# Optimization experiments

Hardware: AMD Instinct MI355X
Metric: run time of the kernel (lower is better)

Reference implementation:

```python
import jax, jax.numpy as jnp
import numpy as np

K = 16          # knn neighbors (init kwarg k)
GROUPS = 4      # GroupNorm groups
EPS = 1e-5
SLOPE = 0.2     # LeakyReLU negative slope


def fps(xyz, n):
    """Farthest point sampling. xyz: (B,N,3) -> idx (B,n). First index is 0 (pointnet2 convention)."""
    B, N, _ = xyz.shape

    def step(carry, _):
        dist, last = carry
        p = jnp.take_along_axis(xyz, last[:, None, None], axis=1)  # (B,1,3)
        d = jnp.sum((xyz - p) ** 2, axis=-1)                       # (B,N)
        dist = jnp.minimum(dist, d)
        nxt = jnp.argmax(dist, axis=-1).astype(jnp.int32)
        return (dist, nxt), nxt

    init = (jnp.full((B, N), jnp.inf, xyz.dtype), jnp.zeros((B,), jnp.int32))
    _, idxs = jax.lax.scan(step, init, None, length=n - 1)  # (n-1, B)
    return jnp.concatenate([jnp.zeros((B, 1), jnp.int32), idxs.T], axis=1)


def graph_feature(cq, fq, ck, fk):
    """DGCNN edge features. cq:(B,Q,3) fq:(B,Q,C) ck:(B,N,3) fk:(B,N,C) -> (B,Q,K,2C)."""
    d2 = (jnp.sum(cq * cq, -1)[:, :, None]
          - 2.0 * jnp.einsum('bqc,bnc->bqn', cq, ck)
          + jnp.sum(ck * ck, -1)[:, None, :])        # (B,Q,N)
    _, idx = jax.lax.top_k(-d2, K)                    # (B,Q,K) nearest first
    nb = jax.vmap(lambda f_, i_: f_[i_])(fk, idx)     # (B,Q,K,C)
    ctr = jnp.broadcast_to(fq[:, :, None, :], nb.shape)
    return jnp.concatenate([nb - ctr, ctr], axis=-1)


def conv_gn_lrelu(y, W, gw, gb):
    """1x1 Conv2d (no bias) + GroupNorm(4) + LeakyReLU(0.2). y: (B,Q,K,Cin), W: (Cout,Cin)."""
    y = jnp.einsum('bqkc,oc->bqko', y, W)
    B, Q, Kk, C = y.shape
    yg = y.reshape(B, Q * Kk, GROUPS, C // GROUPS)
    m = yg.mean(axis=(1, 3), keepdims=True)
    v = yg.var(axis=(1, 3), keepdims=True)
    y = ((yg - m) * jax.lax.rsqrt(v + EPS)).reshape(B, Q, Kk, C) * gw + gb
    return jnp.where(y > 0, y, SLOPE * y)


def setup_inputs() -> dict:
    key = jax.random.key(0)
    ks = jax.random.split(key, 16)
    B, N = 8, 4096
    s = lambda k_, shape, scale=0.1: (jax.random.normal(k_, shape, jnp.float32) * scale)
    return {
        'x': jax.random.normal(ks[0], (B, N, 7), jnp.float32),
        'W_in': s(ks[1], (8, 3), 0.5), 'b_in': s(ks[2], (8,), 0.02),
        'W1': s(ks[3], (32, 16), 0.2), 'g1w': jnp.ones((32,), jnp.float32), 'g1b': jnp.zeros((32,), jnp.float32),
        'W2': s(ks[4], (64, 64), 0.1), 'g2w': jnp.ones((64,), jnp.float32), 'g2b': jnp.zeros((64,), jnp.float32),
        'W3': s(ks[5], (64, 128), 0.1), 'g3w': jnp.ones((64,), jnp.float32), 'g3b': jnp.zeros((64,), jnp.float32),
        'W4': s(ks[6], (128, 128), 0.1), 'g4w': jnp.ones((128,), jnp.float32), 'g4b': jnp.zeros((128,), jnp.float32),
        'num0': 1024,
    }


def reference(x, W_in, b_in, W1, g1w, g1b, W2, g2w, g2b, W3, g3w, g3b, W4, g4w, g4b, num0):
    coor, normal, plane = x[..., :3], x[..., 3:6], x[..., 6:7]   # (B,N,3),(B,N,3),(B,N,1)

    # input_trans: Conv1d(3,8,1)
    f = jnp.einsum('bnc,oc->bno', coor, W_in) + b_in             # (B,N,8)

    g = graph_feature(coor, f, coor, f)                          # (B,N,K,16)
    f = conv_gn_lrelu(g, W1, g1w, g1b).max(axis=2)               # (B,N,32)

    idx = fps(coor, num0)
    gather = lambda a: jnp.take_along_axis(a, idx[:, :, None], axis=1)
    coor_q, normal_q, plane_q, f_q = gather(coor), gather(normal), gather(plane), gather(f)

    g = graph_feature(coor_q, f_q, coor, f)                      # (B,num0,K,64)
    f = conv_gn_lrelu(g, W2, g2w, g2b).max(axis=2)               # (B,num0,64)
    coor, normal, plane = coor_q, normal_q, plane_q

    g = graph_feature(coor, f, coor, f)                          # (B,num0,K,128)
    f = conv_gn_lrelu(g, W3, g3w, g3b).max(axis=2)               # (B,num0,64)

    idx = fps(coor, num0)  # source uses num[0] again
    gather = lambda a: jnp.take_along_axis(a, idx[:, :, None], axis=1)
    coor_q, normal_q, plane_q, f_q = gather(coor), gather(normal), gather(plane), gather(f)

    g = graph_feature(coor_q, f_q, coor, f)                      # (B,num0,K,128)
    f = conv_gn_lrelu(g, W4, g4w, g4b).max(axis=2)               # (B,num0,128)

    return coor_q, f, normal_q, plane_q
```

## Files before the change

kernel.cpp:

```cpp
#include <hip/hip_runtime.h>
#include <cstdint>

static constexpr int B   = 8;
static constexpr int N0  = 4096;
static constexpr int NQ  = 1024;
static constexpr int KNB = 16;

__device__ __forceinline__ unsigned long long wave_max_u64_l63(unsigned long long k) {
#define STEPU_(ctrl)                                                                    \
  {                                                                                     \
    unsigned lo_ = (unsigned)k, hi_ = (unsigned)(k >> 32);                              \
    unsigned plo_ = (unsigned)__builtin_amdgcn_update_dpp((int)lo_, (int)lo_, ctrl,     \
                                                          0xf, 0xf, false);             \
    unsigned phi_ = (unsigned)__builtin_amdgcn_update_dpp((int)hi_, (int)hi_, ctrl,     \
                                                          0xf, 0xf, false);             \
    unsigned long long pk_ = ((unsigned long long)phi_ << 32) | plo_;                   \
    if (pk_ > k) k = pk_;                                                               \
  }
  STEPU_(0x111) STEPU_(0x112) STEPU_(0x114) STEPU_(0x118) STEPU_(0x142) STEPU_(0x143)
#undef STEPU_
  return k;
}

__global__ void prep_kernel(const float* __restrict__ x,
                            const float* __restrict__ W_in,
                            const float* __restrict__ b_in,
                            float4* __restrict__ c4, float* __restrict__ nrm,
                            float* __restrict__ pl, float* __restrict__ f0) {
  int i = blockIdx.x * 256 + threadIdx.x;
  if (i >= B * N0) return;
  const float* xp = x + (size_t)i * 7;
  float cx = xp[0], cy = xp[1], cz = xp[2];
  float kk = __fadd_rn(__fadd_rn(__fmul_rn(cx, cx), __fmul_rn(cy, cy)), __fmul_rn(cz, cz));
  c4[i] = make_float4(cx, cy, cz, kk);
  nrm[i * 3 + 0] = xp[3]; nrm[i * 3 + 1] = xp[4]; nrm[i * 3 + 2] = xp[5];
  pl[i] = xp[6];
#pragma unroll
  for (int o = 0; o < 8; o++) {
    f0[(size_t)i * 8 + o] = cx * W_in[o * 3 + 0] + cy * W_in[o * 3 + 1] + cz * W_in[o * 3 + 2] + b_in[o];
  }
}

template <int NC>
__device__ __forceinline__ void knn_body(int bq, int lane,
                                         const float4* __restrict__ q4,
                                         const float4* __restrict__ k4,
                                         int Q, int Nk, int* __restrict__ out) {
  int b = bq / Q;
  float4 q = q4[bq];
  const float4* kb = k4 + (size_t)b * Nk + lane;
  const float INF    = __int_as_float(0x7f800000);
  const float NEGINF = __int_as_float(0xff800000);
  float myd = INF;
  int   myi = 0;
  float kth = INF;
  const bool isl0 = (lane & 15) == 0;
  constexpr int G = (NC >= 8) ? 8 : NC;
  for (int c0 = 0; c0 < NC; c0 += G) {
    float dg[G];
#pragma unroll
    for (int u = 0; u < G; u++) {
      float4 kp = kb[(c0 + u) * 64];
      float dot = __fadd_rn(__fadd_rn(__fmul_rn(q.x, kp.x), __fmul_rn(q.y, kp.y)),
                            __fmul_rn(q.z, kp.z));
      dg[u] = __fadd_rn(__fsub_rn(q.w, __fmul_rn(2.0f, dot)), kp.w);
    }
#pragma unroll
    for (int u = 0; u < G; u++) {
      float d = dg[u];
      unsigned long long m = __ballot(d < kth);
      while (m) {
        int j = __builtin_ctzll(m);
        float dv = __int_as_float(__builtin_amdgcn_readlane(__float_as_int(d), j));
        int   iv = (c0 + u) * 64 + j;
        bool gt = (myd > dv);
        float pd = __int_as_float(__builtin_amdgcn_update_dpp(
            0, __float_as_int(myd), 0x111, 0xf, 0xf, true));
        int   pi = __builtin_amdgcn_update_dpp(0, myi, 0x111, 0xf, 0xf, true);
        pd = isl0 ? NEGINF : pd;
        bool tp = (pd > dv);
        float nd = tp ? pd : dv;
        int   ni = tp ? pi : iv;
        myd = gt ? nd : myd;
        myi = gt ? ni : myi;
        kth = __int_as_float(__builtin_amdgcn_readlane(__float_as_int(myd), 15));
        m = __ballot(d < kth);
        m = (j < 63) ? (m & (~0ull << (j + 1))) : 0ull;
      }
    }
  }
  if (lane < KNB) out[(size_t)bq * KNB + lane] = myi;
}

template <int CF, int CO>
__device__ __forceinline__ void ctry_body(int i, int total, const float* __restrict__ fq,
                                          const float* __restrict__ W,
                                          float* __restrict__ ctrY,
                                          const int* __restrict__ ridx, int Q, int Nsrc) {
  if (i >= total) return;
  int o = i % CO, bq = i / CO;
  const float* fp;
  if (ridx) {
    int b = bq / Q;
    fp = fq + ((size_t)b * Nsrc + ridx[bq]) * CF;
  } else {
    fp = fq + (size_t)bq * CF;
  }
  const float* wp = W + (size_t)o * (2 * CF) + CF;
  float acc = 0.f;
#pragma unroll
  for (int c = 0; c < CF; c++) acc = fmaf(fp[c], wp[c], acc);
  ctrY[i] = acc;
}

template <int NPTS>
__device__ __forceinline__ void fps_body(const float4* __restrict__ cb, int* w) {
  constexpr int BLK = 256;
  constexpr int M = NPTS / BLK;
  constexpr int NW = BLK / 64;
  __shared__ __align__(16) float2 sxy[NPTS];
  __shared__ float szz[NPTS];
  __shared__ __align__(16) unsigned long long skey[2][NW];
  const int tid = threadIdx.x;
  const int wid = tid >> 6, lane = tid & 63;
  float cx[M], cy[M], cz[M], dist[M];
#pragma unroll
  for (int i = 0; i < M; i++) {
    float4 p = cb[tid * M + i];
    cx[i] = p.x; cy[i] = p.y; cz[i] = p.z;
    dist[i] = 3.4e38f;
    sxy[tid * M + i] = make_float2(p.x, p.y);
    szz[tid * M + i] = p.z;
  }
  w[0] = w[1] = w[2] = w[3] = 0;
  float4 p0 = cb[0];
  float px = p0.x, py = p0.y, pz = p0.z;
  __syncthreads();
  for (int t = 1; t < NQ; t++) {
    float bv = -1.f; int bi = 0;
#pragma unroll
    for (int i = 0; i < M; i++) {
      float dx = __fsub_rn(cx[i], px), dy = __fsub_rn(cy[i], py), dz = __fsub_rn(cz[i], pz);
      float d = __fadd_rn(__fadd_rn(__fmul_rn(dx, dx), __fmul_rn(dy, dy)), __fmul_rn(dz, dz));
      float dd = dist[i]; dd = (d < dd) ? d : dd; dist[i] = dd;
      if (dd > bv) { bv = dd; bi = tid * M + i; }
    }
    unsigned long long k =
        ((unsigned long long)__float_as_uint(bv) << 12) | (unsigned)(4095 - bi);
    k = wave_max_u64_l63(k);
    int p = t & 1;
    if (lane == 63) skey[p][wid] = k;
    __syncthreads();
    ulonglong2 ab = *(const ulonglong2*)&skey[p][0];
    ulonglong2 cd = *(const ulonglong2*)&skey[p][2];
    unsigned long long m0 = (ab.x > ab.y) ? ab.x : ab.y;
    unsigned long long m1 = (cd.x > cd.y) ? cd.x : cd.y;
    unsigned long long mk = (m0 > m1) ? m0 : m1;
    int win = 4095 - (int)(mk & 0xFFFull);
    float2 pxy = sxy[win];
    px = pxy.x; py = pxy.y; pz = szz[win];
    if (t == tid) w[0] = win;
    if (t == tid + 256) w[1] = win;
    if (t == tid + 512) w[2] = win;
    if (t == tid + 768) w[3] = win;
  }
}

__global__ __launch_bounds__(256, 2) void mega1_kernel(
    const float4* __restrict__ c40, const float* __restrict__ nrm,
    const float* __restrict__ pl, const float* __restrict__ f0,
    const float* __restrict__ W1, int* __restrict__ idx1,
    float4* __restrict__ c4q1, float* __restrict__ nq1, float* __restrict__ pq1,
    int* __restrict__ knn1, float* __restrict__ ctrY1) {
  int blk = blockIdx.x;
  if (blk < 8) {
    const int b = blk, tid = threadIdx.x;
    const float4* cb = c40 + (size_t)b * N0;
    int w[4];
    fps_body<N0>(cb, w);
    int* idxb = idx1 + (size_t)b * NQ;
#pragma unroll
    for (int u = 0; u < 4; u++) {
      int r = tid + u * 256;
      int s = (u == 0 && tid == 0) ? 0 : w[u];
      idxb[r] = s;
      c4q1[(size_t)b * NQ + r] = cb[s];
      const float* np = nrm + ((size_t)b * N0 + s) * 3;
      float* ndp = nq1 + ((size_t)b * NQ + r) * 3;
      ndp[0] = np[0]; ndp[1] = np[1]; ndp[2] = np[2];
      pq1[(size_t)b * NQ + r] = pl[(size_t)b * N0 + s];
    }
  } else if (blk < 8 + 8192) {
    int bq = (blk - 8) * 4 + (threadIdx.x >> 6);
    knn_body<64>(bq, threadIdx.x & 63, c40, c40, N0, N0, knn1);
  } else {
    int i = (blk - (8 + 8192)) * 256 + threadIdx.x;
    ctry_body<8, 32>(i, B * N0 * 32, f0, W1, ctrY1, nullptr, 0, 0);
  }
}

__global__ __launch_bounds__(256, 2) void mega2_kernel(
    const float4* __restrict__ c40, const float4* __restrict__ c4q1,
    const float* __restrict__ nq1, const float* __restrict__ pq1,
    const float* __restrict__ f1, const int* __restrict__ idx1,
    const float* __restrict__ W2, int* __restrict__ idx2,
    float4* __restrict__ c4q2, float* __restrict__ cq2out,
    float* __restrict__ nq2out, float* __restrict__ pq2out,
    int* __restrict__ knn2, int* __restrict__ knn3, float* __restrict__ ctrY2) {
  int blk = blockIdx.x;
  if (blk < 8) {
    const int b = blk, tid = threadIdx.x;
    const float4* cqb = c4q1 + (size_t)b * NQ;
    int w[4];
    fps_body<NQ>(cqb, w);
    int* idxb = idx2 + (size_t)b * NQ;
#pragma unroll
    for (int u = 0; u < 4; u++) {
      int r = tid + u * 256;
      int s = (u == 0 && tid == 0) ? 0 : w[u];
      idxb[r] = s;
      float4 c = cqb[s];
      c4q2[(size_t)b * NQ + r] = c;
      float* cd = cq2out + ((size_t)b * NQ + r) * 3;
      cd[0] = c.x; cd[1] = c.y; cd[2] = c.z;
      const float* np = nq1 + ((size_t)b * NQ + s) * 3;
      float* ndp = nq2out + ((size_t)b * NQ + r) * 3;
      ndp[0] = np[0]; ndp[1] = np[1]; ndp[2] = np[2];
      pq2out[(size_t)b * NQ + r] = pq1[(size_t)b * NQ + s];
    }
  } else if (blk < 8 + 2048) {
    int bq = (blk - 8) * 4 + (threadIdx.x >> 6);
    knn_body<64>(bq, threadIdx.x & 63, c4q1, c40, NQ, N0, knn2);
  } else if (blk < 8 + 4096) {
    int bq = (blk - (8 + 2048)) * 4 + (threadIdx.x >> 6);
    knn_body<16>(bq, threadIdx.x & 63, c4q1, c4q1, NQ, NQ, knn3);
  } else {
    int i = (blk - (8 + 4096)) * 256 + threadIdx.x;
    ctry_body<32, 64>(i, B * NQ * 64, f1, W2, ctrY2, idx1, NQ, N0);
  }
}

__global__ __launch_bounds__(256, 4) void mega3_kernel(
    const float4* __restrict__ c4q1, const float4* __restrict__ c4q2,
    const float* __restrict__ f3, const int* __restrict__ idx2,
    const float* __restrict__ W4, int* __restrict__ knn4, float* __restrict__ ctrY4) {
  int blk = blockIdx.x;
  if (blk < 2048) {
    int bq = blk * 4 + (threadIdx.x >> 6);
    knn_body<16>(bq, threadIdx.x & 63, c4q2, c4q1, NQ, NQ, knn4);
  } else {
    int i = (blk - 2048) * 256 + threadIdx.x;
    ctry_body<64, 128>(i, B * NQ * 128, f3, W4, ctrY4, idx2, NQ, NQ);
  }
}

template <int CF, int CO>
__global__ void ctry_kernel(const float* __restrict__ fq, const float* __restrict__ W,
                            float* __restrict__ ctrY, int total) {
  int i = blockIdx.x * 256 + threadIdx.x;
  ctry_body<CF, CO>(i, total, fq, W, ctrY, nullptr, 0, 0);
}

template <int CF, int CO>
__global__ __launch_bounds__(256) void edgeconv_kernel(
    const float* __restrict__ fq, const float* __restrict__ fk,
    const int* __restrict__ knn, const float* __restrict__ Wfull,
    const float* __restrict__ ctrY, const int* __restrict__ ridx,
    float* __restrict__ ymin, float* __restrict__ ymax,
    float* __restrict__ gstats, int Q, int Nk) {
  constexpr int J = CO / 4;
  constexpr int SEC = J * CF + 8;
  __shared__ float Wl[4 * SEC];
  __shared__ float sstat[8];
  for (int t = threadIdx.x; t < CO * CF; t += 256) {
    int o = t / CF, c = t % CF;
    Wl[(o / J) * SEC + (o % J) * CF + c] = Wfull[(size_t)o * (2 * CF) + c];
  }
  if (threadIdx.x < 8) sstat[threadIdx.x] = 0.0f;
  __syncthreads();
  const int wid = threadIdx.x >> 6, lane = threadIdx.x & 63;
  const int bq = blockIdx.x * 4 + wid;
  const int b = bq / Q;
  const int g = lane >> 4, k = lane & 15;
  const int ni = knn[(size_t)bq * KNB + k];
  const float* nbp = fk + (size_t)(b * Nk + ni) * CF;
  const float* cp = ridx ? fq + ((size_t)b * Nk + ridx[bq]) * CF
                         : fq + (size_t)bq * CF;
  float acc[J];
#pragma unroll
  for (int j = 0; j < J; j++) acc[j] = 0.0f;
  const float* wg = &Wl[g * SEC];
#pragma unroll
  for (int c = 0; c < CF; c += 4) {
    float4 nb4 = *(const float4*)(nbp + c);
    float4 c4  = *(const float4*)(cp + c);
    float e0 = nb4.x - c4.x, e1 = nb4.y - c4.y, e2 = nb4.z - c4.z, e3 = nb4.w - c4.w;
#pragma unroll
    for (int j = 0; j < J; j++) {
      float4 w4 = *(const float4*)(wg + j * CF + c);
      acc[j] = fmaf(e0, w4.x, acc[j]);
      acc[j] = fmaf(e1, w4.y, acc[j]);
      acc[j] = fmaf(e2, w4.z, acc[j]);
      acc[j] = fmaf(e3, w4.w, acc[j]);
    }
  }
  float s = 0.f, s2 = 0.f;
  const float* cyp = ctrY + (size_t)bq * CO + g * J;
#pragma unroll
  for (int j = 0; j < J; j++) {
    float y = acc[j] + cyp[j];
    acc[j] = y;
    s += y; s2 = fmaf(y, y, s2);
  }
  float mn[J];
#pragma unroll
  for (int j = 0; j < J; j++) mn[j] = acc[j];
#pragma unroll
  for (int m = 1; m < 16; m <<= 1) {
#pragma unroll
    for (int j = 0; j < J; j++) {
      float a = __shfl_xor(acc[j], m); if (a > acc[j]) acc[j] = a;
      float c2 = __shfl_xor(mn[j], m); if (c2 < mn[j]) mn[j] = c2;
    }
    s  += __shfl_xor(s, m);
    s2 += __shfl_xor(s2, m);
  }
  if (k == 0) {
    float* mnp = ymin + (size_t)bq * CO + g * J;
    float* mxp = ymax + (size_t)bq * CO + g * J;
#pragma unroll
    for (int j = 0; j < J; j++) { mnp[j] = mn[j]; mxp[j] = acc[j]; }
    atomicAdd(&sstat[g], s);
    atomicAdd(&sstat[4 + g], s2);
  }
  __syncthreads();
  if (threadIdx.x < 8) atomicAdd(&gstats[b * 8 + threadIdx.x], sstat[threadIdx.x]);
}

template <int CO>
__global__ void gn_out_kernel(const float* __restrict__ ymin, const float* __restrict__ ymax,
                              const float* __restrict__ gstats, const float* __restrict__ gw,
                              const float* __restrict__ gb, float* __restrict__ fout,
                              int total, int Q, float inv_cnt) {
  int i = blockIdx.x * 256 + threadIdx.x;
  if (i >= total) return;
  constexpr int J = CO / 4;
  int o = i % CO; int bq = i / CO; int b = bq / Q;
  int g = o / J;
  float m  = gstats[b * 8 + g] * inv_cnt;
  float s2 = gstats[b * 8 + 4 + g] * inv_cnt;
  float rs = rsqrtf(s2 - m * m + 1e-5f);
  float sc = gw[o] * rs;
  float sel = (sc >= 0.f) ? ymax[i] : ymin[i];
  float v = (sel - m) * sc + gb[o];
  fout[i] = (v > 0.f) ? v : 0.2f * v;
}

extern "C" void kernel_launch(void* const* d_in, const int* in_sizes, int n_in,
                              void* d_out, int out_size, void* d_ws, size_t ws_size,
                              hipStream_t stream) {
  (void)in_sizes; (void)n_in; (void)out_size; (void)ws_size;
  const float* x    = (const float*)d_in[0];
  const float* W_in = (const float*)d_in[1];
  const float* b_in = (const float*)d_in[2];
  const float* W1   = (const float*)d_in[3];
  const float* g1w  = (const float*)d_in[4];
  const float* g1b  = (const float*)d_in[5];
  const float* W2   = (const float*)d_in[6];
  const float* g2w  = (const float*)d_in[7];
  const float* g2b  = (const float*)d_in[8];
  const float* W3   = (const float*)d_in[9];
  const float* g3w  = (const float*)d_in[10];
  const float* g3b  = (const float*)d_in[11];
  const float* W4   = (const float*)d_in[12];
  const float* g4w  = (const float*)d_in[13];
  const float* g4b  = (const float*)d_in[14];

  float* ws = (float*)d_ws;
  size_t o_c40  = 0;
  size_t o_nrm  = o_c40  + (size_t)B * N0 * 4;
  size_t o_pl   = o_nrm  + (size_t)B * N0 * 3;
  size_t o_f0   = o_pl   + (size_t)B * N0;
  size_t o_f1   = o_f0   + (size_t)B * N0 * 8;
  size_t o_ctrY = o_f1   + (size_t)B * N0 * 32;
  size_t o_ymin = o_ctrY + (size_t)B * N0 * 32;
  size_t o_ymax = o_ymin + (size_t)B * N0 * 32;
  size_t o_knnA = o_ymax + (size_t)B * N0 * 32;
  size_t o_knnB = o_knnA + (size_t)B * N0 * KNB;
  size_t o_gst  = o_knnB + (size_t)B * NQ * KNB;
  size_t o_idx1 = o_gst  + 4 * B * 8;
  size_t o_idx2 = o_idx1 + (size_t)B * NQ;
  size_t o_c4q1 = o_idx2 + (size_t)B * NQ;
  size_t o_c4q2 = o_c4q1 + (size_t)B * NQ * 4;
  size_t o_nq1  = o_c4q2 + (size_t)B * NQ * 4;
  size_t o_pq1  = o_nq1  + (size_t)B * NQ * 3;
  size_t o_f2   = o_pq1  + (size_t)B * NQ;
  size_t o_f3   = o_f2   + (size_t)B * NQ * 64;

  float4* c40  = (float4*)(ws + o_c40);
  float*  nrm  = ws + o_nrm;   float* pl   = ws + o_pl;
  float*  f0   = ws + o_f0;    float* f1   = ws + o_f1;
  float*  ctrY = ws + o_ctrY;  float* ymin = ws + o_ymin;  float* ymax = ws + o_ymax;
  int*    knnA = (int*)(ws + o_knnA);
  int*    knnB = (int*)(ws + o_knnB);
  float*  gst  = ws + o_gst;
  int*    idx1 = (int*)(ws + o_idx1);
  int*    idx2 = (int*)(ws + o_idx2);
  float4* c4q1 = (float4*)(ws + o_c4q1);
  float4* c4q2 = (float4*)(ws + o_c4q2);
  float*  nq1  = ws + o_nq1;   float* pq1  = ws + o_pq1;
  float*  f2   = ws + o_f2;    float* f3   = ws + o_f3;

  float* out  = (float*)d_out;
  float* cq2  = out;
  float* fout = out + (size_t)B * NQ * 3;
  float* nq2  = fout + (size_t)B * NQ * 128;
  float* pq2  = nq2 + (size_t)B * NQ * 3;

  hipMemsetAsync(gst, 0, 4 * B * 8 * sizeof(float), stream);

  prep_kernel<<<(B * N0 + 255) / 256, 256, 0, stream>>>(x, W_in, b_in, c40, nrm, pl, f0);

  mega1_kernel<<<8 + 8192 + 4096, 256, 0, stream>>>(c40, nrm, pl, f0, W1,
                                                    idx1, c4q1, nq1, pq1, knnA, ctrY);
  edgeconv_kernel<8, 32><<<B * N0 / 4, 256, 0, stream>>>(f0, f0, knnA, W1, ctrY, nullptr,
                                                         ymin, ymax, gst + 0, N0, N0);
  gn_out_kernel<32><<<(B * N0 * 32 + 255) / 256, 256, 0, stream>>>(
      ymin, ymax, gst + 0, g1w, g1b, f1, B * N0 * 32, N0, 1.0f / (4096.0f * 16.0f * 8.0f));

  mega2_kernel<<<8 + 2048 + 2048 + 2048, 256, 0, stream>>>(
      c40, c4q1, nq1, pq1, f1, idx1, W2, idx2, c4q2, cq2, nq2, pq2, knnA, knnB, ctrY);
  edgeconv_kernel<32, 64><<<B * NQ / 4, 256, 0, stream>>>(f1, f1, knnA, W2, ctrY, idx1,
                                                          ymin, ymax, gst + B * 8, NQ, N0);
  gn_out_kernel<64><<<(B * NQ * 64 + 255) / 256, 256, 0, stream>>>(
      ymin, ymax, gst + B * 8, g2w, g2b, f2, B * NQ * 64, NQ, 1.0f / (1024.0f * 16.0f * 16.0f));

  ctry_kernel<64, 64><<<(B * NQ * 64 + 255) / 256, 256, 0, stream>>>(f2, W3, ctrY, B * NQ * 64);
  edgeconv_kernel<64, 64><<<B * NQ / 4, 256, 0, stream>>>(f2, f2, knnB, W3, ctrY, nullptr,
                                                          ymin, ymax, gst + 2 * B * 8, NQ, NQ);
  gn_out_kernel<64><<<(B * NQ * 64 + 255) / 256, 256, 0, stream>>>(
      ymin, ymax, gst + 2 * B * 8, g3w, g3b, f3, B * NQ * 64, NQ, 1.0f / (1024.0f * 16.0f * 16.0f));

  mega3_kernel<<<2048 + 4096, 256, 0, stream>>>(c4q1, c4q2, f3, idx2, W4, knnB, ctrY);
  edgeconv_kernel<64, 128><<<B * NQ / 4, 256, 0, stream>>>(f3, f3, knnB, W4, ctrY, idx2,
                                                           ymin, ymax, gst + 3 * B * 8, NQ, NQ);
  gn_out_kernel<128><<<(B * NQ * 128 + 255) / 256, 256, 0, stream>>>(
      ymin, ymax, gst + 3 * B * 8, g4w, g4b, fout, B * NQ * 128, NQ, 1.0f / (1024.0f * 16.0f * 32.0f));
}
```

Baseline: 1.508 ms.

## Batch FPS over multiple clouds per block, carry coords in reduction, move FPS2 earlier

FPS now processes two clouds per block (four for the second FPS), interleaving independent reductions so one barrier per iteration is shared across several batches. The winning point's coordinates travel through the DPP wave reduction, which removes the shared-memory point table and the dependent LDS lookup after each step. The second FPS moves out of mega2 and is fused with the first edgeconv launch, so it starts earlier and overlaps edgeconv1 and gn_out. In exchange, fewer blocks carry the serial FPS critical path, each with more registers and work per iteration.

```diff
diff --git a/kernel.cpp b/kernel.cpp
--- a/kernel.cpp
+++ b/kernel.cpp
@@ -6,20 +6,31 @@
 static constexpr int NQ  = 1024;
 static constexpr int KNB = 16;
 
-__device__ __forceinline__ unsigned long long wave_max_u64_l63(unsigned long long k) {
-#define STEPU_(ctrl)                                                                    \
-  {                                                                                     \
-    unsigned lo_ = (unsigned)k, hi_ = (unsigned)(k >> 32);                              \
-    unsigned plo_ = (unsigned)__builtin_amdgcn_update_dpp((int)lo_, (int)lo_, ctrl,     \
-                                                          0xf, 0xf, false);             \
-    unsigned phi_ = (unsigned)__builtin_amdgcn_update_dpp((int)hi_, (int)hi_, ctrl,     \
-                                                          0xf, 0xf, false);             \
-    unsigned long long pk_ = ((unsigned long long)phi_ << 32) | plo_;                   \
-    if (pk_ > k) k = pk_;                                                               \
-  }
-  STEPU_(0x111) STEPU_(0x112) STEPU_(0x114) STEPU_(0x118) STEPU_(0x142) STEPU_(0x143)
-#undef STEPU_
-  return k;
+__device__ __forceinline__ void wave_max_u64_xyz_l63(unsigned long long& k,
+                                                     float& x, float& y, float& z) {
+#define STEPP_(ctrl)                                                                     \
+  {                                                                                      \
+    unsigned lo_ = (unsigned)k, hi_ = (unsigned)(k >> 32);                               \
+    unsigned plo_ = (unsigned)__builtin_amdgcn_update_dpp((int)lo_, (int)lo_, ctrl,      \
+                                                          0xf, 0xf, false);              \
+    unsigned phi_ = (unsigned)__builtin_amdgcn_update_dpp((int)hi_, (int)hi_, ctrl,      \
+                                                          0xf, 0xf, false);              \
+    float px_ = __int_as_float(__builtin_amdgcn_update_dpp(__float_as_int(x),            \
+                                                           __float_as_int(x), ctrl,     \
+                                                           0xf, 0xf, false));            \
+    float py_ = __int_as_float(__builtin_amdgcn_update_dpp(__float_as_int(y),            \
+                                                           __float_as_int(y), ctrl,     \
+                                                           0xf, 0xf, false));            \
+    float pz_ = __int_as_float(__builtin_amdgcn_update_dpp(__float_as_int(z),            \
+                                                           __float_as_int(z), ctrl,     \
+                                                           0xf, 0xf, false));            \
+    unsigned long long pk_ = ((unsigned long long)phi_ << 32) | plo_;                    \
+    bool sw_ = pk_ > k;                                                                  \
+    k = sw_ ? pk_ : k;                                                                   \
+    x = sw_ ? px_ : x; y = sw_ ? py_ : y; z = sw_ ? pz_ : z;                             \
+  }
+  STEPP_(0x111) STEPP_(0x112) STEPP_(0x114) STEPP_(0x118) STEPP_(0x142) STEPP_(0x143)
+#undef STEPP_
 }
 
 __global__ void prep_kernel(const float* __restrict__ x,
@@ -113,57 +124,151 @@
   ctrY[i] = acc;
 }
 
-template <int NPTS>
-__device__ __forceinline__ void fps_body(const float4* __restrict__ cb, int* w) {
-  constexpr int BLK = 256;
-  constexpr int M = NPTS / BLK;
-  constexpr int NW = BLK / 64;
-  __shared__ __align__(16) float2 sxy[NPTS];
-  __shared__ float szz[NPTS];
-  __shared__ __align__(16) unsigned long long skey[2][NW];
+template <int NPTS, int BPB>
+__device__ __forceinline__ void fps_body_multi(const float4* __restrict__ cb,
+                                               int (&w)[BPB][4]) {
+  constexpr int M = NPTS / 256;
+  __shared__ __align__(16) unsigned long long skey[2][BPB][4];
+  __shared__ __align__(16) float4 spay[2][BPB][4];
   const int tid = threadIdx.x;
   const int wid = tid >> 6, lane = tid & 63;
-  float cx[M], cy[M], cz[M], dist[M];
-#pragma unroll
-  for (int i = 0; i < M; i++) {
-    float4 p = cb[tid * M + i];
-    cx[i] = p.x; cy[i] = p.y; cz[i] = p.z;
-    dist[i] = 3.4e38f;
-    sxy[tid * M + i] = make_float2(p.x, p.y);
-    szz[tid * M + i] = p.z;
-  }
-  w[0] = w[1] = w[2] = w[3] = 0;
-  float4 p0 = cb[0];
-  float px = p0.x, py = p0.y, pz = p0.z;
+  float cx[BPB][M], cy[BPB][M], cz[BPB][M], dist[BPB][M];
+  float px[BPB], py[BPB], pz[BPB];
+#pragma unroll
+  for (int bb = 0; bb < BPB; bb++) {
+#pragma unroll
+    for (int i = 0; i < M; i++) {
+      float4 p = cb[(size_t)bb * NPTS + tid * M + i];
+      cx[bb][i] = p.x; cy[bb][i] = p.y; cz[bb][i] = p.z;
+      dist[bb][i] = 3.4e38f;
+    }
+#pragma unroll
+    for (int u = 0; u < 4; u++) w[bb][u] = 0;
+    float4 p0 = cb[(size_t)bb * NPTS];
+    px[bb] = p0.x; py[bb] = p0.y; pz[bb] = p0.z;
+  }
+  for (int t = 1; t < NQ; t++) {
+    const int p = t & 1;
+#pragma unroll
+    for (int bb = 0; bb < BPB; bb++) {
+      float bv = -1.f; int bi = 0;
+      float bx = 0.f, by = 0.f, bz = 0.f;
+#pragma unroll
+      for (int i = 0; i < M; i++) {
+        float dx = __fsub_rn(cx[bb][i], px[bb]);
+        float dy = __fsub_rn(cy[bb][i], py[bb]);
+        float dz = __fsub_rn(cz[bb][i], pz[bb]);
+        float d = __fadd_rn(__fadd_rn(__fmul_rn(dx, dx), __fmul_rn(dy, dy)), __fmul_rn(dz, dz));
+        float dd = dist[bb][i]; dd = (d < dd) ? d : dd; dist[bb][i] = dd;
+        if (dd > bv) { bv = dd; bi = tid * M + i; bx = cx[bb][i]; by = cy[bb][i]; bz = cz[bb][i]; }
+      }
+      unsigned long long k =
+          ((unsigned long long)__float_as_uint(bv) << 12) | (unsigned)(4095 - bi);
+      wave_max_u64_xyz_l63(k, bx, by, bz);
+      if (lane == 63) {
+        skey[p][bb][wid] = k;
+        spay[p][bb][wid] = make_float4(bx, by, bz, 0.f);
+      }
+    }
+    __syncthreads();
+#pragma unroll
+    for (int bb = 0; bb < BPB; bb++) {
+      unsigned long long k0 = skey[p][bb][0], k1 = skey[p][bb][1];
+      unsigned long long k2 = skey[p][bb][2], k3 = skey[p][bb][3];
+      float4 q0 = spay[p][bb][0], q1 = spay[p][bb][1];
+      float4 q2 = spay[p][bb][2], q3 = spay[p][bb][3];
+      bool sA = k1 > k0;
+      unsigned long long ka = sA ? k1 : k0;
+      float xa = sA ? q1.x : q0.x, ya = sA ? q1.y : q0.y, za = sA ? q1.z : q0.z;
+      bool sB = k3 > k2;
+      unsigned long long kb2 = sB ? k3 : k2;
+      float xb = sB ? q3.x : q2.x, yb = sB ? q3.y : q2.y, zb = sB ? q3.z : q2.z;
+      bool sC = kb2 > ka;
+      unsigned long long kw = sC ? kb2 : ka;
+      px[bb] = sC ? xb : xa; py[bb] = sC ? yb : ya; pz[bb] = sC ? zb : za;
+      int win = 4095 - (int)(kw & 0xFFFull);
+      if (t == tid) w[bb][0] = win;
+      if (t == tid + 256) w[bb][1] = win;
+      if (t == tid + 512) w[bb][2] = win;
+      if (t == tid + 768) w[bb][3] = win;
+    }
+  }
+}
+
+template <int CF, int CO>
+__device__ __forceinline__ void edgeconv_body(
+    int blkid, const float* __restrict__ fq, const float* __restrict__ fk,
+    const int* __restrict__ knn, const float* __restrict__ Wfull,
+    const float* __restrict__ ctrY, const int* __restrict__ ridx,
+    float* __restrict__ ymin, float* __restrict__ ymax,
+    float* __restrict__ gstats, int Q, int Nk) {
+  constexpr int J = CO / 4;
+  constexpr int SEC = J * CF + 8;
+  __shared__ float Wl[4 * SEC];
+  __shared__ float sstat[8];
+  for (int t = threadIdx.x; t < CO * CF; t += 256) {
+    int o = t / CF, c = t % CF;
+    Wl[(o / J) * SEC + (o % J) * CF + c] = Wfull[(size_t)o * (2 * CF) + c];
+  }
+  if (threadIdx.x < 8) sstat[threadIdx.x] = 0.0f;
   __syncthreads();
-  for (int t = 1; t < NQ; t++) {
-    float bv = -1.f; int bi = 0;
-#pragma unroll
-    for (int i = 0; i < M; i++) {
-      float dx = __fsub_rn(cx[i], px), dy = __fsub_rn(cy[i], py), dz = __fsub_rn(cz[i], pz);
-      float d = __fadd_rn(__fadd_rn(__fmul_rn(dx, dx), __fmul_rn(dy, dy)), __fmul_rn(dz, dz));
-      float dd = dist[i]; dd = (d < dd) ? d : dd; dist[i] = dd;
-      if (dd > bv) { bv = dd; bi = tid * M + i; }
-    }
-    unsigned long long k =
-        ((unsigned long long)__float_as_uint(bv) << 12) | (unsigned)(4095 - bi);
-    k = wave_max_u64_l63(k);
-    int p = t & 1;
-    if (lane == 63) skey[p][wid] = k;
-    __syncthreads();
-    ulonglong2 ab = *(const ulonglong2*)&skey[p][0];
-    ulonglong2 cd = *(const ulonglong2*)&skey[p][2];
-    unsigned long long m0 = (ab.x > ab.y) ? ab.x : ab.y;
-    unsigned long long m1 = (cd.x > cd.y) ? cd.x : cd.y;
-    unsigned long long mk = (m0 > m1) ? m0 : m1;
-    int win = 4095 - (int)(mk & 0xFFFull);
-    float2 pxy = sxy[win];
-    px = pxy.x; py = pxy.y; pz = szz[win];
-    if (t == tid) w[0] = win;
-    if (t == tid + 256) w[1] = win;
-    if (t == tid + 512) w[2] = win;
-    if (t == tid + 768) w[3] = win;
-  }
+  const int wid = threadIdx.x >> 6, lane = threadIdx.x & 63;
+  const int bq = blkid * 4 + wid;
+  const int b = bq / Q;
+  const int g = lane >> 4, k = lane & 15;
+  const int ni = knn[(size_t)bq * KNB + k];
+  const float* nbp = fk + (size_t)(b * Nk + ni) * CF;
+  const float* cp = ridx ? fq + ((size_t)b * Nk + ridx[bq]) * CF
+                         : fq + (size_t)bq * CF;
+  float acc[J];
+#pragma unroll
+  for (int j = 0; j < J; j++) acc[j] = 0.0f;
+  const float* wg = &Wl[g * SEC];
+#pragma unroll
+  for (int c = 0; c < CF; c += 4) {
+    float4 nb4 = *(const float4*)(nbp + c);
+    float4 c4  = *(const float4*)(cp + c);
+    float e0 = nb4.x - c4.x, e1 = nb4.y - c4.y, e2 = nb4.z - c4.z, e3 = nb4.w - c4.w;
+#pragma unroll
+    for (int j = 0; j < J; j++) {
+      float4 w4 = *(const float4*)(wg + j * CF + c);
+      acc[j] = fmaf(e0, w4.x, acc[j]);
+      acc[j] = fmaf(e1, w4.y, acc[j]);
+      acc[j] = fmaf(e2, w4.z, acc[j]);
+      acc[j] = fmaf(e3, w4.w, acc[j]);
+    }
+  }
+  float s = 0.f, s2 = 0.f;
+  const float* cyp = ctrY + (size_t)bq * CO + g * J;
+#pragma unroll
+  for (int j = 0; j < J; j++) {
+    float y = acc[j] + cyp[j];
+    acc[j] = y;
+    s += y; s2 = fmaf(y, y, s2);
+  }
+  float mn[J];
+#pragma unroll
+  for (int j = 0; j < J; j++) mn[j] = acc[j];
+#pragma unroll
+  for (int m = 1; m < 16; m <<= 1) {
+#pragma unroll
+    for (int j = 0; j < J; j++) {
+      float a = __shfl_xor(acc[j], m); if (a > acc[j]) acc[j] = a;
+      float c2 = __shfl_xor(mn[j], m); if (c2 < mn[j]) mn[j] = c2;
+    }
+    s  += __shfl_xor(s, m);
+    s2 += __shfl_xor(s2, m);
+  }
+  if (k == 0) {
+    float* mnp = ymin + (size_t)bq * CO + g * J;
+    float* mxp = ymax + (size_t)bq * CO + g * J;
+#pragma unroll
+    for (int j = 0; j < J; j++) { mnp[j] = mn[j]; mxp[j] = acc[j]; }
+    atomicAdd(&sstat[g], s);
+    atomicAdd(&sstat[4 + g], s2);
+  }
+  __syncthreads();
+  if (threadIdx.x < 8) atomicAdd(&gstats[b * 8 + threadIdx.x], sstat[threadIdx.x]);
 }
 
 __global__ __launch_bounds__(256, 2) void mega1_kernel(
@@ -173,69 +278,94 @@
     float4* __restrict__ c4q1, float* __restrict__ nq1, float* __restrict__ pq1,
     int* __restrict__ knn1, float* __restrict__ ctrY1) {
   int blk = blockIdx.x;
-  if (blk < 8) {
-    const int b = blk, tid = threadIdx.x;
-    const float4* cb = c40 + (size_t)b * N0;
-    int w[4];
-    fps_body<N0>(cb, w);
-    int* idxb = idx1 + (size_t)b * NQ;
-#pragma unroll
-    for (int u = 0; u < 4; u++) {
-      int r = tid + u * 256;
-      int s = (u == 0 && tid == 0) ? 0 : w[u];
-      idxb[r] = s;
-      c4q1[(size_t)b * NQ + r] = cb[s];
-      const float* np = nrm + ((size_t)b * N0 + s) * 3;
-      float* ndp = nq1 + ((size_t)b * NQ + r) * 3;
-      ndp[0] = np[0]; ndp[1] = np[1]; ndp[2] = np[2];
-      pq1[(size_t)b * NQ + r] = pl[(size_t)b * N0 + s];
-    }
-  } else if (blk < 8 + 8192) {
-    int bq = (blk - 8) * 4 + (threadIdx.x >> 6);
+  if (blk < 4) {
+    const int tid = threadIdx.x;
+    const int b0 = blk * 2;
+    const float4* cb = c40 + (size_t)b0 * N0;
+    int w[2][4];
+    fps_body_multi<N0, 2>(cb, w);
+#pragma unroll
+    for (int bb = 0; bb < 2; bb++) {
+      const int b = b0 + bb;
+      const float4* cbb = c40 + (size_t)b * N0;
+      int* idxb = idx1 + (size_t)b * NQ;
+#pragma unroll
+      for (int u = 0; u < 4; u++) {
+        int r = tid + u * 256;
+        int s = (u == 0 && tid == 0) ? 0 : w[bb][u];
+        idxb[r] = s;
+        c4q1[(size_t)b * NQ + r] = cbb[s];
+        const float* np = nrm + ((size_t)b * N0 + s) * 3;
+        float* ndp = nq1 + ((size_t)b * NQ + r) * 3;
+        ndp[0] = np[0]; ndp[1] = np[1]; ndp[2] = np[2];
+        pq1[(size_t)b * NQ + r] = pl[(size_t)b * N0 + s];
+      }
+    }
+  } else if (blk < 4 + 8192) {
+    int bq = (blk - 4) * 4 + (threadIdx.x >> 6);
     knn_body<64>(bq, threadIdx.x & 63, c40, c40, N0, N0, knn1);
   } else {
-    int i = (blk - (8 + 8192)) * 256 + threadIdx.x;
+    int i = (blk - (4 + 8192)) * 256 + threadIdx.x;
     ctry_body<8, 32>(i, B * N0 * 32, f0, W1, ctrY1, nullptr, 0, 0);
+  }
+}
+
+__global__ __launch_bounds__(256) void ec1f_kernel(
+    const float4* __restrict__ c4q1, const float* __restrict__ nq1,
+    const float* __restrict__ pq1, const float* __restrict__ f0,
+    const int* __restrict__ knn1, const float* __restrict__ W1,
+    const float* __restrict__ ctrY1, float* __restrict__ ymin,
+    float* __restrict__ ymax, float* __restrict__ gst1,
+    int* __restrict__ idx2, float4* __restrict__ c4q2,
+    float* __restrict__ cq2out, float* __restrict__ nq2out,
+    float* __restrict__ pq2out) {
+  int blk = blockIdx.x;
+  if (blk < 2) {
+    const int tid = threadIdx.x;
+    const int b0 = blk * 4;
+    const float4* cqb = c4q1 + (size_t)b0 * NQ;
+    int w[4][4];
+    fps_body_multi<NQ, 4>(cqb, w);
+#pragma unroll
+    for (int bb = 0; bb < 4; bb++) {
+      const int b = b0 + bb;
+      const float4* cbb = c4q1 + (size_t)b * NQ;
+      int* idxb = idx2 + (size_t)b * NQ;
+#pragma unroll
+      for (int u = 0; u < 4; u++) {
+        int r = tid + u * 256;
+        int s = (u == 0 && tid == 0) ? 0 : w[bb][u];
+        idxb[r] = s;
+        float4 c = cbb[s];
+        c4q2[(size_t)b * NQ + r] = c;
+        float* cd = cq2out + ((size_t)b * NQ + r) * 3;
+        cd[0] = c.x; cd[1] = c.y; cd[2] = c.z;
+        const float* np = nq1 + ((size_t)b * NQ + s) * 3;
+        float* ndp = nq2out + ((size_t)b * NQ + r) * 3;
+        ndp[0] = np[0]; ndp[1] = np[1]; ndp[2] = np[2];
+        pq2out[(size_t)b * NQ + r] = pq1[(size_t)b * NQ + s];
+      }
+    }
+  } else {
+    edgeconv_body<8, 32>(blk - 2, f0, f0, knn1, W1, ctrY1, nullptr,
+                         ymin, ymax, gst1, N0, N0);
   }
 }
 
 __global__ __launch_bounds__(256, 2) void mega2_kernel(
     const float4* __restrict__ c40, const float4* __restrict__ c4q1,
-    const float* __restrict__ nq1, const float* __restrict__ pq1,
     const float* __restrict__ f1, const int* __restrict__ idx1,
-    const float* __restrict__ W2, int* __restrict__ idx2,
-    float4* __restrict__ c4q2, float* __restrict__ cq2out,
-    float* __restrict__ nq2out, float* __restrict__ pq2out,
+    const float* __restrict__ W2,
     int* __restrict__ knn2, int* __restrict__ knn3, float* __restrict__ ctrY2) {
   int blk = blockIdx.x;
-  if (blk < 8) {
-    const int b = blk, tid = threadIdx.x;
-    const float4* cqb = c4q1 + (size_t)b * NQ;
-    int w[4];
-    fps_body<NQ>(cqb, w);
-    int* idxb = idx2 + (size_t)b * NQ;
-#pragma unroll
-    for (int u = 0; u < 4; u++) {
-      int r = tid + u * 256;
-      int s = (u == 0 && tid == 0) ? 0 : w[u];
-      idxb[r] = s;
-      float4 c = cqb[s];
-      c4q2[(size_t)b * NQ + r] = c;
-      float* cd = cq2out + ((size_t)b * NQ + r) * 3;
-      cd[0] = c.x; cd[1] = c.y; cd[2] = c.z;
-      const float* np = nq1 + ((size_t)b * NQ + s) * 3;
-      float* ndp = nq2out + ((size_t)b * NQ + r) * 3;
-      ndp[0] = np[0]; ndp[1] = np[1]; ndp[2] = np[2];
-      pq2out[(size_t)b * NQ + r] = pq1[(size_t)b * NQ + s];
-    }
-  } else if (blk < 8 + 2048) {
-    int bq = (blk - 8) * 4 + (threadIdx.x >> 6);
+  if (blk < 2048) {
+    int bq = blk * 4 + (threadIdx.x >> 6);
     knn_body<64>(bq, threadIdx.x & 63, c4q1, c40, NQ, N0, knn2);
-  } else if (blk < 8 + 4096) {
-    int bq = (blk - (8 + 2048)) * 4 + (threadIdx.x >> 6);
+  } else if (blk < 4096) {
+    int bq = (blk - 2048) * 4 + (threadIdx.x >> 6);
     knn_body<16>(bq, threadIdx.x & 63, c4q1, c4q1, NQ, NQ, knn3);
   } else {
-    int i = (blk - (8 + 4096)) * 256 + threadIdx.x;
+    int i = (blk - 4096) * 256 + threadIdx.x;
     ctry_body<32, 64>(i, B * NQ * 64, f1, W2, ctrY2, idx1, NQ, N0);
   }
 }
@@ -268,73 +398,8 @@
     const float* __restrict__ ctrY, const int* __restrict__ ridx,
     float* __restrict__ ymin, float* __restrict__ ymax,
     float* __restrict__ gstats, int Q, int Nk) {
-  constexpr int J = CO / 4;
-  constexpr int SEC = J * CF + 8;
-  __shared__ float Wl[4 * SEC];
-  __shared__ float sstat[8];
-  for (int t = threadIdx.x; t < CO * CF; t += 256) {
-    int o = t / CF, c = t % CF;
-    Wl[(o / J) * SEC + (o % J) * CF + c] = Wfull[(size_t)o * (2 * CF) + c];
-  }
-  if (threadIdx.x < 8) sstat[threadIdx.x] = 0.0f;
-  __syncthreads();
-  const int wid = threadIdx.x >> 6, lane = threadIdx.x & 63;
-  const int bq = blockIdx.x * 4 + wid;
-  const int b = bq / Q;
-  const int g = lane >> 4, k = lane & 15;
-  const int ni = knn[(size_t)bq * KNB + k];
-  const float* nbp = fk + (size_t)(b * Nk + ni) * CF;
-  const float* cp = ridx ? fq + ((size_t)b * Nk + ridx[bq]) * CF
-                         : fq + (size_t)bq * CF;
-  float acc[J];
-#pragma unroll
-  for (int j = 0; j < J; j++) acc[j] = 0.0f;
-  const float* wg = &Wl[g * SEC];
-#pragma unroll
-  for (int c = 0; c < CF; c += 4) {
-    float4 nb4 = *(const float4*)(nbp + c);
-    float4 c4  = *(const float4*)(cp + c);
-    float e0 = nb4.x - c4.x, e1 = nb4.y - c4.y, e2 = nb4.z - c4.z, e3 = nb4.w - c4.w;
-#pragma unroll
-    for (int j = 0; j < J; j++) {
-      float4 w4 = *(const float4*)(wg + j * CF + c);
-      acc[j] = fmaf(e0, w4.x, acc[j]);
-      acc[j] = fmaf(e1, w4.y, acc[j]);
-      acc[j] = fmaf(e2, w4.z, acc[j]);
-      acc[j] = fmaf(e3, w4.w, acc[j]);
-    }
-  }
-  float s = 0.f, s2 = 0.f;
-  const float* cyp = ctrY + (size_t)bq * CO + g * J;
-#pragma unroll
-  for (int j = 0; j < J; j++) {
-    float y = acc[j] + cyp[j];
-    acc[j] = y;
-    s += y; s2 = fmaf(y, y, s2);
-  }
-  float mn[J];
-#pragma unroll
-  for (int j = 0; j < J; j++) mn[j] = acc[j];
-#pragma unroll
-  for (int m = 1; m < 16; m <<= 1) {
-#pragma unroll
-    for (int j = 0; j < J; j++) {
-      float a = __shfl_xor(acc[j], m); if (a > acc[j]) acc[j] = a;
-      float c2 = __shfl_xor(mn[j], m); if (c2 < mn[j]) mn[j] = c2;
-    }
-    s  += __shfl_xor(s, m);
-    s2 += __shfl_xor(s2, m);
-  }
-  if (k == 0) {
-    float* mnp = ymin + (size_t)bq * CO + g * J;
-    float* mxp = ymax + (size_t)bq * CO + g * J;
-#pragma unroll
-    for (int j = 0; j < J; j++) { mnp[j] = mn[j]; mxp[j] = acc[j]; }
-    atomicAdd(&sstat[g], s);
-    atomicAdd(&sstat[4 + g], s2);
-  }
-  __syncthreads();
-  if (threadIdx.x < 8) atomicAdd(&gstats[b * 8 + threadIdx.x], sstat[threadIdx.x]);
+  edgeconv_body<CF, CO>(blockIdx.x, fq, fk, knn, Wfull, ctrY, ridx,
+                        ymin, ymax, gstats, Q, Nk);
 }
 
 template <int CO>
@@ -421,15 +486,16 @@
 
   prep_kernel<<<(B * N0 + 255) / 256, 256, 0, stream>>>(x, W_in, b_in, c40, nrm, pl, f0);
 
-  mega1_kernel<<<8 + 8192 + 4096, 256, 0, stream>>>(c40, nrm, pl, f0, W1,
+  mega1_kernel<<<4 + 8192 + 4096, 256, 0, stream>>>(c40, nrm, pl, f0, W1,
                                                     idx1, c4q1, nq1, pq1, knnA, ctrY);
-  edgeconv_kernel<8, 32><<<B * N0 / 4, 256, 0, stream>>>(f0, f0, knnA, W1, ctrY, nullptr,
-                                                         ymin, ymax, gst + 0, N0, N0);
+  ec1f_kernel<<<2 + 8192, 256, 0, stream>>>(c4q1, nq1, pq1, f0, knnA, W1, ctrY,
+                                            ymin, ymax, gst + 0,
+                                            idx2, c4q2, cq2, nq2, pq2);
   gn_out_kernel<32><<<(B * N0 * 32 + 255) / 256, 256, 0, stream>>>(
       ymin, ymax, gst + 0, g1w, g1b, f1, B * N0 * 32, N0, 1.0f / (4096.0f * 16.0f * 8.0f));
 
-  mega2_kernel<<<8 + 2048 + 2048 + 2048, 256, 0, stream>>>(
-      c40, c4q1, nq1, pq1, f1, idx1, W2, idx2, c4q2, cq2, nq2, pq2, knnA, knnB, ctrY);
+  mega2_kernel<<<2048 + 2048 + 2048, 256, 0, stream>>>(
+      c40, c4q1, f1, idx1, W2, knnA, knnB, ctrY);
   edgeconv_kernel<32, 64><<<B * NQ / 4, 256, 0, stream>>>(f1, f1, knnA, W2, ctrY, idx1,
                                                           ymin, ymax, gst + B * 8, NQ, N0);
   gn_out_kernel<64><<<(B * NQ * 64 + 255) / 256, 256, 0, stream>>>(
```

Result: slower. 4.380 ms (+190.5%).

## Replace FPS block barrier with tagged LDS spin and overlap second FPS with edgeconv1

Applied to the files above, without the earlier changes.

Each FPS iteration's __syncthreads is replaced by an iteration-tagged atomic store plus a spin-load over the four wave keys in LDS, so each wave proceeds as soon as all four keys for this step are published. The second FPS, which depends only on the first FPS output, moves out of mega2 into a new kernel that also runs the first edgeconv, letting that serial FPS overlap with edgeconv1 blocks. The aim is to shorten the serial FPS critical path and hide it behind parallel work. The risk is that spin-waiting waves burn issue slots, and correctness relies on the tag (t<<44) comparisons and on only two parity slots being used.

```diff
diff --git a/kernel.cpp b/kernel.cpp
--- a/kernel.cpp
+++ b/kernel.cpp
@@ -114,13 +114,11 @@
 }
 
 template <int NPTS>
-__device__ __forceinline__ void fps_body(const float4* __restrict__ cb, int* w) {
-  constexpr int BLK = 256;
-  constexpr int M = NPTS / BLK;
-  constexpr int NW = BLK / 64;
+__device__ __forceinline__ void fps_body(const float4* __restrict__ cb, int (&w)[4]) {
+  constexpr int M = NPTS / 256;
   __shared__ __align__(16) float2 sxy[NPTS];
   __shared__ float szz[NPTS];
-  __shared__ __align__(16) unsigned long long skey[2][NW];
+  __shared__ __align__(16) unsigned long long skey[2][4];
   const int tid = threadIdx.x;
   const int wid = tid >> 6, lane = tid & 63;
   float cx[M], cy[M], cz[M], dist[M];
@@ -132,6 +130,7 @@
     sxy[tid * M + i] = make_float2(p.x, p.y);
     szz[tid * M + i] = p.z;
   }
+  if (tid < 8) skey[tid >> 2][tid & 3] = 0ull;
   w[0] = w[1] = w[2] = w[3] = 0;
   float4 p0 = cb[0];
   float px = p0.x, py = p0.y, pz = p0.z;
@@ -148,14 +147,21 @@
     unsigned long long k =
         ((unsigned long long)__float_as_uint(bv) << 12) | (unsigned)(4095 - bi);
     k = wave_max_u64_l63(k);
-    int p = t & 1;
-    if (lane == 63) skey[p][wid] = k;
-    __syncthreads();
-    ulonglong2 ab = *(const ulonglong2*)&skey[p][0];
-    ulonglong2 cd = *(const ulonglong2*)&skey[p][2];
-    unsigned long long m0 = (ab.x > ab.y) ? ab.x : ab.y;
-    unsigned long long m1 = (cd.x > cd.y) ? cd.x : cd.y;
-    unsigned long long mk = (m0 > m1) ? m0 : m1;
+    const int par = t & 1;
+    const unsigned long long tagbase = (unsigned long long)t << 44;
+    if (lane == 63)
+      __hip_atomic_store(&skey[par][wid], k | tagbase,
+                         __ATOMIC_RELAXED, __HIP_MEMORY_SCOPE_WORKGROUP);
+    unsigned long long k0, k1, k2, k3;
+    do {
+      k0 = __hip_atomic_load(&skey[par][0], __ATOMIC_RELAXED, __HIP_MEMORY_SCOPE_WORKGROUP);
+      k1 = __hip_atomic_load(&skey[par][1], __ATOMIC_RELAXED, __HIP_MEMORY_SCOPE_WORKGROUP);
+      k2 = __hip_atomic_load(&skey[par][2], __ATOMIC_RELAXED, __HIP_MEMORY_SCOPE_WORKGROUP);
+      k3 = __hip_atomic_load(&skey[par][3], __ATOMIC_RELAXED, __HIP_MEMORY_SCOPE_WORKGROUP);
+    } while (k0 < tagbase || k1 < tagbase || k2 < tagbase || k3 < tagbase);
+    unsigned long long m0 = (k1 > k0) ? k1 : k0;
+    unsigned long long m1 = (k3 > k2) ? k3 : k2;
+    unsigned long long mk = (m1 > m0) ? m1 : m0;
     int win = 4095 - (int)(mk & 0xFFFull);
     float2 pxy = sxy[win];
     px = pxy.x; py = pxy.y; pz = szz[win];
@@ -164,6 +170,83 @@
     if (t == tid + 512) w[2] = win;
     if (t == tid + 768) w[3] = win;
   }
+}
+
+template <int CF, int CO, int NT>
+__device__ __forceinline__ void edgeconv_body(
+    int blkid, const float* __restrict__ fq, const float* __restrict__ fk,
+    const int* __restrict__ knn, const float* __restrict__ Wfull,
+    const float* __restrict__ ctrY, const int* __restrict__ ridx,
+    float* __restrict__ ymin, float* __restrict__ ymax,
+    float* __restrict__ gstats, int Q, int Nk) {
+  constexpr int J = CO / 4;
+  constexpr int SEC = J * CF + 8;
+  constexpr int NWARP = NT / 64;
+  __shared__ float Wl[4 * SEC];
+  __shared__ float sstat[8];
+  for (int t = threadIdx.x; t < CO * CF; t += NT) {
+    int o = t / CF, c = t % CF;
+    Wl[(o / J) * SEC + (o % J) * CF + c] = Wfull[(size_t)o * (2 * CF) + c];
+  }
+  if (threadIdx.x < 8) sstat[threadIdx.x] = 0.0f;
+  __syncthreads();
+  const int wid = threadIdx.x >> 6, lane = threadIdx.x & 63;
+  const int bq = blkid * NWARP + wid;
+  const int b = bq / Q;
+  const int g = lane >> 4, k = lane & 15;
+  const int ni = knn[(size_t)bq * KNB + k];
+  const float* nbp = fk + (size_t)(b * Nk + ni) * CF;
+  const float* cp = ridx ? fq + ((size_t)b * Nk + ridx[bq]) * CF
+                         : fq + (size_t)bq * CF;
+  float acc[J];
+#pragma unroll
+  for (int j = 0; j < J; j++) acc[j] = 0.0f;
+  const float* wg = &Wl[g * SEC];
+#pragma unroll
+  for (int c = 0; c < CF; c += 4) {
+    float4 nb4 = *(const float4*)(nbp + c);
+    float4 c4  = *(const float4*)(cp + c);
+    float e0 = nb4.x - c4.x, e1 = nb4.y - c4.y, e2 = nb4.z - c4.z, e3 = nb4.w - c4.w;
+#pragma unroll
+    for (int j = 0; j < J; j++) {
+      float4 w4 = *(const float4*)(wg + j * CF + c);
+      acc[j] = fmaf(e0, w4.x, acc[j]);
+      acc[j] = fmaf(e1, w4.y, acc[j]);
+      acc[j] = fmaf(e2, w4.z, acc[j]);
+      acc[j] = fmaf(e3, w4.w, acc[j]);
+    }
+  }
+  float s = 0.f, s2 = 0.f;
+  const float* cyp = ctrY + (size_t)bq * CO + g * J;
+#pragma unroll
+  for (int j = 0; j < J; j++) {
+    float y = acc[j] + cyp[j];
+    acc[j] = y;
+    s += y; s2 = fmaf(y, y, s2);
+  }
+  float mn[J];
+#pragma unroll
+  for (int j = 0; j < J; j++) mn[j] = acc[j];
+#pragma unroll
+  for (int m = 1; m < 16; m <<= 1) {
+#pragma unroll
+    for (int j = 0; j < J; j++) {
+      float a = __shfl_xor(acc[j], m); if (a > acc[j]) acc[j] = a;
+      float c2 = __shfl_xor(mn[j], m); if (c2 < mn[j]) mn[j] = c2;
+    }
+    s  += __shfl_xor(s, m);
+    s2 += __shfl_xor(s2, m);
+  }
+  if (k == 0) {
+    float* mnp = ymin + (size_t)bq * CO + g * J;
+    float* mxp = ymax + (size_t)bq * CO + g * J;
+#pragma unroll
+    for (int j = 0; j < J; j++) { mnp[j] = mn[j]; mxp[j] = acc[j]; }
+    atomicAdd(&sstat[g], s);
+    atomicAdd(&sstat[4 + g], s2);
+  }
+  __syncthreads();
+  if (threadIdx.x < 8) atomicAdd(&gstats[b * 8 + threadIdx.x], sstat[threadIdx.x]);
 }
 
 __global__ __launch_bounds__(256, 2) void mega1_kernel(
@@ -199,14 +282,15 @@
   }
 }
 
-__global__ __launch_bounds__(256, 2) void mega2_kernel(
-    const float4* __restrict__ c40, const float4* __restrict__ c4q1,
-    const float* __restrict__ nq1, const float* __restrict__ pq1,
-    const float* __restrict__ f1, const int* __restrict__ idx1,
-    const float* __restrict__ W2, int* __restrict__ idx2,
-    float4* __restrict__ c4q2, float* __restrict__ cq2out,
-    float* __restrict__ nq2out, float* __restrict__ pq2out,
-    int* __restrict__ knn2, int* __restrict__ knn3, float* __restrict__ ctrY2) {
+__global__ __launch_bounds__(256, 2) void ec1f_kernel(
+    const float4* __restrict__ c4q1, const float* __restrict__ nq1,
+    const float* __restrict__ pq1, const float* __restrict__ f0,
+    const int* __restrict__ knn1, const float* __restrict__ W1,
+    const float* __restrict__ ctrY1, float* __restrict__ ymin,
+    float* __restrict__ ymax, float* __restrict__ gst1,
+    int* __restrict__ idx2, float4* __restrict__ c4q2,
+    float* __restrict__ cq2out, float* __restrict__ nq2out,
+    float* __restrict__ pq2out) {
   int blk = blockIdx.x;
   if (blk < 8) {
     const int b = blk, tid = threadIdx.x;
@@ -228,14 +312,26 @@
       ndp[0] = np[0]; ndp[1] = np[1]; ndp[2] = np[2];
       pq2out[(size_t)b * NQ + r] = pq1[(size_t)b * NQ + s];
     }
-  } else if (blk < 8 + 2048) {
-    int bq = (blk - 8) * 4 + (threadIdx.x >> 6);
+  } else {
+    edgeconv_body<8, 32, 256>(blk - 8, f0, f0, knn1, W1, ctrY1, nullptr,
+                              ymin, ymax, gst1, N0, N0);
+  }
+}
+
+__global__ __launch_bounds__(256, 2) void mega2_kernel(
+    const float4* __restrict__ c40, const float4* __restrict__ c4q1,
+    const float* __restrict__ f1, const int* __restrict__ idx1,
+    const float* __restrict__ W2,
+    int* __restrict__ knn2, int* __restrict__ knn3, float* __restrict__ ctrY2) {
+  int blk = blockIdx.x;
+  if (blk < 2048) {
+    int bq = blk * 4 + (threadIdx.x >> 6);
     knn_body<64>(bq, threadIdx.x & 63, c4q1, c40, NQ, N0, knn2);
-  } else if (blk < 8 + 4096) {
-    int bq = (blk - (8 + 2048)) * 4 + (threadIdx.x >> 6);
+  } else if (blk < 4096) {
+    int bq = (blk - 2048) * 4 + (threadIdx.x >> 6);
     knn_body<16>(bq, threadIdx.x & 63, c4q1, c4q1, NQ, NQ, knn3);
   } else {
-    int i = (blk - (8 + 4096)) * 256 + threadIdx.x;
+    int i = (blk - 4096) * 256 + threadIdx.x;
     ctry_body<32, 64>(i, B * NQ * 64, f1, W2, ctrY2, idx1, NQ, N0);
   }
 }
@@ -268,73 +364,8 @@
     const float* __restrict__ ctrY, const int* __restrict__ ridx,
     float* __restrict__ ymin, float* __restrict__ ymax,
     float* __restrict__ gstats, int Q, int Nk) {
-  constexpr int J = CO / 4;
-  constexpr int SEC = J * CF + 8;
-  __shared__ float Wl[4 * SEC];
-  __shared__ float sstat[8];
-  for (int t = threadIdx.x; t < CO * CF; t += 256) {
-    int o = t / CF, c = t % CF;
-    Wl[(o / J) * SEC + (o % J) * CF + c] = Wfull[(size_t)o * (2 * CF) + c];
-  }
-  if (threadIdx.x < 8) sstat[threadIdx.x] = 0.0f;
-  __syncthreads();
-  const int wid = threadIdx.x >> 6, lane = threadIdx.x & 63;
-  const int bq = blockIdx.x * 4 + wid;
-  const int b = bq / Q;
-  const int g = lane >> 4, k = lane & 15;
-  const int ni = knn[(size_t)bq * KNB + k];
-  const float* nbp = fk + (size_t)(b * Nk + ni) * CF;
-  const float* cp = ridx ? fq + ((size_t)b * Nk + ridx[bq]) * CF
-                         : fq + (size_t)bq * CF;
-  float acc[J];
-#pragma unroll
-  for (int j = 0; j < J; j++) acc[j] = 0.0f;
-  const float* wg = &Wl[g * SEC];
-#pragma unroll
-  for (int c = 0; c < CF; c += 4) {
-    float4 nb4 = *(const float4*)(nbp + c);
-    float4 c4  = *(const float4*)(cp + c);
-    float e0 = nb4.x - c4.x, e1 = nb4.y - c4.y, e2 = nb4.z - c4.z, e3 = nb4.w - c4.w;
-#pragma unroll
-    for (int j = 0; j < J; j++) {
-      float4 w4 = *(const float4*)(wg + j * CF + c);
-      acc[j] = fmaf(e0, w4.x, acc[j]);
-      acc[j] = fmaf(e1, w4.y, acc[j]);
-      acc[j] = fmaf(e2, w4.z, acc[j]);
-      acc[j] = fmaf(e3, w4.w, acc[j]);
-    }
-  }
-  float s = 0.f, s2 = 0.f;
-  const float* cyp = ctrY + (size_t)bq * CO + g * J;
-#pragma unroll
-  for (int j = 0; j < J; j++) {
-    float y = acc[j] + cyp[j];
-    acc[j] = y;
-    s += y; s2 = fmaf(y, y, s2);
-  }
-  float mn[J];
-#pragma unroll
-  for (int j = 0; j < J; j++) mn[j] = acc[j];
-#pragma unroll
-  for (int m = 1; m < 16; m <<= 1) {
-#pragma unroll
-    for (int j = 0; j < J; j++) {
-      float a = __shfl_xor(acc[j], m); if (a > acc[j]) acc[j] = a;
-      float c2 = __shfl_xor(mn[j], m); if (c2 < mn[j]) mn[j] = c2;
-    }
-    s  += __shfl_xor(s, m);
-    s2 += __shfl_xor(s2, m);
-  }
-  if (k == 0) {
-    float* mnp = ymin + (size_t)bq * CO + g * J;
-    float* mxp = ymax + (size_t)bq * CO + g * J;
-#pragma unroll
-    for (int j = 0; j < J; j++) { mnp[j] = mn[j]; mxp[j] = acc[j]; }
-    atomicAdd(&sstat[g], s);
-    atomicAdd(&sstat[4 + g], s2);
-  }
-  __syncthreads();
-  if (threadIdx.x < 8) atomicAdd(&gstats[b * 8 + threadIdx.x], sstat[threadIdx.x]);
+  edgeconv_body<CF, CO, 256>(blockIdx.x, fq, fk, knn, Wfull, ctrY, ridx,
+                             ymin, ymax, gstats, Q, Nk);
 }
 
 template <int CO>
@@ -423,13 +454,14 @@
 
   mega1_kernel<<<8 + 8192 + 4096, 256, 0, stream>>>(c40, nrm, pl, f0, W1,
                                                     idx1, c4q1, nq1, pq1, knnA, ctrY);
-  edgeconv_kernel<8, 32><<<B * N0 / 4, 256, 0, stream>>>(f0, f0, knnA, W1, ctrY, nullptr,
-                                                         ymin, ymax, gst + 0, N0, N0);
+  ec1f_kernel<<<8 + 8192, 256, 0, stream>>>(c4q1, nq1, pq1, f0, knnA, W1, ctrY,
+                                            ymin, ymax, gst + 0,
+                                            idx2, c4q2, cq2, nq2, pq2);
   gn_out_kernel<32><<<(B * N0 * 32 + 255) / 256, 256, 0, stream>>>(
       ymin, ymax, gst + 0, g1w, g1b, f1, B * N0 * 32, N0, 1.0f / (4096.0f * 16.0f * 8.0f));
 
-  mega2_kernel<<<8 + 2048 + 2048 + 2048, 256, 0, stream>>>(
-      c40, c4q1, nq1, pq1, f1, idx1, W2, idx2, c4q2, cq2, nq2, pq2, knnA, knnB, ctrY);
+  mega2_kernel<<<2048 + 2048 + 2048, 256, 0, stream>>>(
+      c40, c4q1, f1, idx1, W2, knnA, knnB, ctrY);
   edgeconv_kernel<32, 64><<<B * NQ / 4, 256, 0, stream>>>(f1, f1, knnA, W2, ctrY, idx1,
                                                           ymin, ymax, gst + B * 8, NQ, N0);
   gn_out_kernel<64><<<(B * NQ * 64 + 255) / 256, 256, 0, stream>>>(
```

Measured after the change: 1.694 ms. 12.4% more time.
